# Kernel optimization log

Hardware: AMD Instinct MI355X
Metric: run time of the kernel (lower is better)

Reference implementation:

```python
import jax, jax.numpy as jnp
import numpy as np

B, S, D_MODEL, N_HEADS = 2, 256, 512, 8
HEAD_DIM = D_MODEL // N_HEADS  # 64; k.size(-1) used for scaling


def setup_inputs() -> dict:
    key = jax.random.key(0)
    ks = jax.random.split(key, 11)
    sd = 1.0 / np.sqrt(D_MODEL)
    sf = 1.0 / np.sqrt(N_HEADS * D_MODEL)
    return {
        "Q": jax.random.normal(ks[0], (B, S, D_MODEL), jnp.float32),
        "K": jax.random.normal(ks[1], (B, S, D_MODEL), jnp.float32),
        "V": jax.random.normal(ks[2], (B, S, D_MODEL), jnp.float32),
        "Wq": jax.random.normal(ks[3], (D_MODEL, D_MODEL * N_HEADS), jnp.float32) * sd,
        "bq": jax.random.normal(ks[4], (D_MODEL * N_HEADS,), jnp.float32) * sd,
        "Wk": jax.random.normal(ks[5], (D_MODEL, D_MODEL * N_HEADS), jnp.float32) * sd,
        "bk": jax.random.normal(ks[6], (D_MODEL * N_HEADS,), jnp.float32) * sd,
        "Wv": jax.random.normal(ks[7], (D_MODEL, D_MODEL * N_HEADS), jnp.float32) * sd,
        "bv": jax.random.normal(ks[8], (D_MODEL * N_HEADS,), jnp.float32) * sd,
        "Wf": jax.random.normal(ks[9], (N_HEADS * D_MODEL, D_MODEL), jnp.float32) * sf,
        "bf": jax.random.normal(ks[10], (D_MODEL,), jnp.float32) * sf,
    }


def _split_heads(x):
    # Faithful to torch: view(B, -1, n_heads, d_model//n_heads).transpose(1, 2).
    # x: (B, S, D_MODEL*N_HEADS) -> (B, N_HEADS, S*N_HEADS, HEAD_DIM)
    b = x.shape[0]
    return jnp.transpose(x.reshape(b, -1, N_HEADS, HEAD_DIM), (0, 2, 1, 3))


def reference(Q, K, V, Wq, bq, Wk, bk, Wv, bv, Wf, bf):
    q = _split_heads(Q @ Wq + bq)  # (B, H, S*H, Dh)
    k = _split_heads(K @ Wk + bk)
    v = _split_heads(V @ Wv + bv)
    scale = 1.0 / jnp.sqrt(jnp.float32(HEAD_DIM))
    scores = jnp.einsum("bhqd,bhkd->bhqk", q, k) * scale  # (B, H, S*H, S*H)
    weights = jax.nn.softmax(scores, axis=-1)
    ctx = jnp.einsum("bhqk,bhkd->bhqd", weights, v)  # (B, H, S*H, Dh)
    # transpose(1,2).view(B, -1, n_heads*d_model) -> (B, S, N_HEADS*D_MODEL)
    ctx = jnp.transpose(ctx, (0, 2, 1, 3)).reshape(Q.shape[0], -1, N_HEADS * D_MODEL)
    return ctx @ Wf + bf  # (B, S, D_MODEL)
```

## Files before the change

kernel.cpp:

```cpp
#include <hip/hip_runtime.h>
#include <hip/hip_bf16.h>


typedef __attribute__((ext_vector_type(4))) float f32x4;
typedef __attribute__((ext_vector_type(8))) short short8;
typedef __attribute__((ext_vector_type(4))) short short4v;

#define SEQ 2048
#define DH 64
#define BH 16
#define ROWS 512
#define DM 512
#define NQ 4096
#define KSPLIT 8

static __device__ __forceinline__ unsigned short f2bf(float f) {
    return __builtin_bit_cast(unsigned short, __float2bfloat16(f));
}
static __device__ __forceinline__ short4v pk4(float a, float b, float c, float d) {
    return short4v{(short)f2bf(a), (short)f2bf(b), (short)f2bf(c), (short)f2bf(d)};
}

__global__ __launch_bounds__(256, 2) void qkv_proj_kernel(
    const float* __restrict__ Q, const float* __restrict__ K, const float* __restrict__ V,
    const float* __restrict__ Wq, const float* __restrict__ bq,
    const float* __restrict__ Wk, const float* __restrict__ bk,
    const float* __restrict__ Wv, const float* __restrict__ bv,
    unsigned short* __restrict__ q_bf, unsigned short* __restrict__ k_bf,
    unsigned short* __restrict__ vT_bf)
{
    const int mat = blockIdx.z;
    const float* X    = (mat == 0) ? Q  : (mat == 1) ? K  : V;
    const float* W    = (mat == 0) ? Wq : (mat == 1) ? Wk : Wv;
    const float* bias = (mat == 0) ? bq : (mat == 1) ? bk : bv;

    const int n0 = blockIdx.x * 64;
    const int m0 = blockIdx.y * 128;
    const int tid = threadIdx.x;
    const int w = tid >> 6, l = tid & 63;
    const int lr = l & 15, lg = l >> 4;

    __shared__ unsigned short a_lds[128][72];
    __shared__ unsigned short wt_lds[64 * 72];

    const int xr0 = tid >> 4, xc4 = (tid & 15) * 4;
    const int wn = tid & 63, wkseg = tid >> 6;
    const int wxr = (wn >> 3) & 7;

    f32x4 acc[2][4];
#pragma unroll
    for (int qh = 0; qh < 2; ++qh)
#pragma unroll
        for (int ct = 0; ct < 4; ++ct) acc[qh][ct] = f32x4{0.f, 0.f, 0.f, 0.f};

    float4 rx[8];
    float rwv[16];

#pragma unroll
    for (int i = 0; i < 8; ++i)
        rx[i] = *reinterpret_cast<const float4*>(X + (m0 + i * 16 + xr0) * DM + xc4);
#pragma unroll
    for (int j = 0; j < 16; ++j)
        rwv[j] = W[(size_t)(wkseg * 16 + j) * NQ + n0 + wn];

    for (int t = 0; t < 8; ++t) {
#pragma unroll
        for (int i = 0; i < 8; ++i)
            *reinterpret_cast<short4v*>(&a_lds[i * 16 + xr0][xc4]) =
                pk4(rx[i].x, rx[i].y, rx[i].z, rx[i].w);
#pragma unroll
        for (int j4 = 0; j4 < 4; ++j4) {
            int kb = wkseg * 2 + (j4 >> 1);
            int off = wn * 72 + ((kb ^ wxr) << 3) + (j4 & 1) * 4;
            *reinterpret_cast<short4v*>(&wt_lds[off]) =
                pk4(rwv[j4 * 4 + 0], rwv[j4 * 4 + 1], rwv[j4 * 4 + 2], rwv[j4 * 4 + 3]);
        }
        __syncthreads();

        if (t < 7) {
            int k0 = (t + 1) * 64;
#pragma unroll
            for (int i = 0; i < 8; ++i)
                rx[i] = *reinterpret_cast<const float4*>(X + (m0 + i * 16 + xr0) * DM + k0 + xc4);
#pragma unroll
            for (int j = 0; j < 16; ++j)
                rwv[j] = W[(size_t)(k0 + wkseg * 16 + j) * NQ + n0 + wn];
        }

#pragma unroll
        for (int ks = 0; ks < 2; ++ks) {
            short8 aA = *reinterpret_cast<const short8*>(&a_lds[w * 32 + lr][ks * 32 + lg * 8]);
            short8 aB = *reinterpret_cast<const short8*>(&a_lds[w * 32 + 16 + lr][ks * 32 + lg * 8]);
#pragma unroll
            for (int ct = 0; ct < 4; ++ct) {
                int row = ct * 16 + lr;
                int kb = ks * 4 + lg;
                short8 b = *reinterpret_cast<const short8*>(
                    &wt_lds[row * 72 + ((kb ^ ((row >> 3) & 7)) << 3)]);
                acc[0][ct] = __builtin_amdgcn_mfma_f32_16x16x32_bf16(aA, b, acc[0][ct], 0, 0, 0);
                acc[1][ct] = __builtin_amdgcn_mfma_f32_16x16x32_bf16(aB, b, acc[1][ct], 0, 0, 0);
            }
        }
        __syncthreads();
    }

#pragma unroll
    for (int ct = 0; ct < 4; ++ct) {
        int c = n0 + ct * 16 + lr;
        float bv_ = bias[c];
        int h = (c >> 6) & 7, d = c & 63, c1 = c >> 9;
#pragma unroll
        for (int qh = 0; qh < 2; ++qh)
#pragma unroll
            for (int r = 0; r < 4; ++r) {
                int row = m0 + w * 32 + qh * 16 + lg * 4 + r;
                int b = row >> 8, s = row & 255;
                int n = s * 8 + c1;
                unsigned short bfv = f2bf(acc[qh][ct][r] + bv_);
                if (mat == 0)      q_bf[((b * 8 + h) * SEQ + n) * DH + d] = bfv;
                else if (mat == 1) k_bf[((b * 8 + h) * SEQ + n) * DH + d] = bfv;
                else               vT_bf[((b * 8 + h) * DH + d) * SEQ + n] = bfv;
            }
    }
}

__global__ __launch_bounds__(512, 4) void attn_kernel(
    const unsigned short* __restrict__ q_bf,
    const unsigned short* __restrict__ k_bf,
    const unsigned short* __restrict__ vT_bf,
    unsigned short* __restrict__ ctx_bf)
{
    const int bh = blockIdx.y;
    const int b = bh >> 3, h = bh & 7;
    const int n0 = blockIdx.x * 64;
    const int tid = threadIdx.x;
    const int w = tid >> 6, l = tid & 63;
    const int wq = w & 3, half = w >> 2;
    const int lr = l & 15, lg = l >> 4;
    const int gtid = tid & 255;

    const unsigned short* qb = q_bf + (size_t)bh * SEQ * DH;
    const unsigned short* kb = k_bf + (size_t)bh * SEQ * DH;
    const unsigned short* vb = vT_bf + (size_t)bh * DH * SEQ;

    __shared__ unsigned short kl[2][64][72];
    __shared__ unsigned short vl[2][64][72];
    __shared__ unsigned short pl[8][16][72];
    __shared__ float o_lds[4][16][68];
    __shared__ float l_lds[4][16];

    const int qrow = n0 + wq * 16 + lr;
    short8 aq[2];
    aq[0] = *reinterpret_cast<const short8*>(qb + qrow * DH + lg * 8);
    aq[1] = *reinterpret_cast<const short8*>(qb + qrow * DH + 32 + lg * 8);

    f32x4 o[4];
    float l_part[4];
#pragma unroll
    for (int i = 0; i < 4; ++i) {
        o[i] = f32x4{0.f, 0.f, 0.f, 0.f};
        l_part[i] = 0.f;
    }

    const int srow = gtid >> 3, sc8 = (gtid & 7) * 8;
    const int kbase0 = half * (SEQ / 2);

    short8 rk[2], rv[2];
#pragma unroll
    for (int i = 0; i < 2; ++i) {
        int row = srow + i * 32;
        rk[i] = *reinterpret_cast<const short8*>(kb + (kbase0 + row) * DH + sc8);
        rv[i] = *reinterpret_cast<const short8*>(vb + row * SEQ + kbase0 + sc8);
    }

    for (int kt = 0; kt < SEQ / 2 / 64; ++kt) {
#pragma unroll
        for (int i = 0; i < 2; ++i) {
            *reinterpret_cast<short8*>(&kl[half][srow + i * 32][sc8]) = rk[i];
            *reinterpret_cast<short8*>(&vl[half][srow + i * 32][sc8]) = rv[i];
        }
        __syncthreads();

        if (kt < SEQ / 2 / 64 - 1) {
            int kb0 = kbase0 + (kt + 1) * 64;
#pragma unroll
            for (int i = 0; i < 2; ++i) {
                int row = srow + i * 32;
                rk[i] = *reinterpret_cast<const short8*>(kb + (kb0 + row) * DH + sc8);
                rv[i] = *reinterpret_cast<const short8*>(vb + row * SEQ + kb0 + sc8);
            }
        }

        f32x4 s[4];
#pragma unroll
        for (int ct = 0; ct < 4; ++ct) s[ct] = f32x4{0.f, 0.f, 0.f, 0.f};
#pragma unroll
        for (int ks = 0; ks < 2; ++ks) {
#pragma unroll
            for (int ct = 0; ct < 4; ++ct) {
                short8 bfrag = *reinterpret_cast<const short8*>(&kl[half][ct * 16 + lr][ks * 32 + lg * 8]);
                s[ct] = __builtin_amdgcn_mfma_f32_16x16x32_bf16(aq[ks], bfrag, s[ct], 0, 0, 0);
            }
        }

#pragma unroll
        for (int r = 0; r < 4; ++r) {
            float rs = 0.f;
#pragma unroll
            for (int ct = 0; ct < 4; ++ct) {
                float p = __expf(s[ct][r] * 0.125f);
                s[ct][r] = p;
                rs += p;
            }
            l_part[r] += rs;
#pragma unroll
            for (int ct = 0; ct < 4; ++ct)
                pl[w][lg * 4 + r][ct * 16 + lr] = f2bf(s[ct][r]);
        }
        asm volatile("s_waitcnt lgkmcnt(0)" ::: "memory");
        __builtin_amdgcn_sched_barrier(0);

#pragma unroll
        for (int ks = 0; ks < 2; ++ks) {
            short8 pa = *reinterpret_cast<const short8*>(&pl[w][lr][ks * 32 + lg * 8]);
#pragma unroll
            for (int dt = 0; dt < 4; ++dt) {
                short8 vfrag = *reinterpret_cast<const short8*>(&vl[half][dt * 16 + lr][ks * 32 + lg * 8]);
                o[dt] = __builtin_amdgcn_mfma_f32_16x16x32_bf16(pa, vfrag, o[dt], 0, 0, 0);
            }
        }
        __syncthreads();
    }

    float lsum[4];
#pragma unroll
    for (int r = 0; r < 4; ++r) {
        float rs = l_part[r];
        rs += __shfl_xor(rs, 1);
        rs += __shfl_xor(rs, 2);
        rs += __shfl_xor(rs, 4);
        rs += __shfl_xor(rs, 8);
        lsum[r] = rs;
    }

    if (half == 1) {
#pragma unroll
        for (int r = 0; r < 4; ++r) {
#pragma unroll
            for (int dt = 0; dt < 4; ++dt)
                o_lds[wq][lg * 4 + r][dt * 16 + lr] = o[dt][r];
            if (lr == 0) l_lds[wq][lg * 4 + r] = lsum[r];
        }
    }
    __syncthreads();
    if (half == 0) {
#pragma unroll
        for (int r = 0; r < 4; ++r) {
            float l_tot = lsum[r] + l_lds[wq][lg * 4 + r];
            float inv = 1.f / l_tot;
            int n = n0 + wq * 16 + lg * 4 + r;
            int sp = n >> 3;
            int cbase = (n & 7) * 512 + h * 64;
#pragma unroll
            for (int dt = 0; dt < 4; ++dt) {
                float ot = o[dt][r] + o_lds[wq][lg * 4 + r][dt * 16 + lr];
                ctx_bf[((size_t)(b * 256 + sp)) * NQ + cbase + dt * 16 + lr] = f2bf(ot * inv);
            }
        }
    }
}

__global__ __launch_bounds__(256) void out_proj_splitk_kernel(
    const unsigned short* __restrict__ ctx_bf,
    const float* __restrict__ Wf,
    float* __restrict__ part)
{
    const int n0 = blockIdx.x * 64;
    const int m0 = blockIdx.y * 64;
    const int ksplit = blockIdx.z;
    const int kbase = ksplit * (NQ / KSPLIT);
    const int tid = threadIdx.x;
    const int w = tid >> 6, l = tid & 63;
    const int lr = l & 15, lg = l >> 4;

    __shared__ unsigned short a_lds[64][72];
    __shared__ unsigned short wt_lds[64 * 72];

    const int arow0 = tid >> 3, ac8 = (tid & 7) * 8;
    const int wn = tid & 63, wkseg = tid >> 6;
    const int wxr = (wn >> 3) & 7;

    f32x4 acc[4];
#pragma unroll
    for (int ct = 0; ct < 4; ++ct) acc[ct] = f32x4{0.f, 0.f, 0.f, 0.f};

    short8 ra[2];
    float rwv[16];

    {
#pragma unroll
        for (int i = 0; i < 2; ++i)
            ra[i] = *reinterpret_cast<const short8*>(
                ctx_bf + (size_t)(m0 + arow0 + i * 32) * NQ + kbase + ac8);
#pragma unroll
        for (int j = 0; j < 16; ++j)
            rwv[j] = Wf[(size_t)(kbase + wkseg * 16 + j) * DM + n0 + wn];
    }

    for (int t = 0; t < 8; ++t) {
#pragma unroll
        for (int i = 0; i < 2; ++i)
            *reinterpret_cast<short8*>(&a_lds[arow0 + i * 32][ac8]) = ra[i];
#pragma unroll
        for (int j4 = 0; j4 < 4; ++j4) {
            int kb = wkseg * 2 + (j4 >> 1);
            int off = wn * 72 + ((kb ^ wxr) << 3) + (j4 & 1) * 4;
            *reinterpret_cast<short4v*>(&wt_lds[off]) =
                pk4(rwv[j4 * 4 + 0], rwv[j4 * 4 + 1], rwv[j4 * 4 + 2], rwv[j4 * 4 + 3]);
        }
        __syncthreads();

        if (t < 7) {
            int k0 = kbase + (t + 1) * 64;
#pragma unroll
            for (int i = 0; i < 2; ++i)
                ra[i] = *reinterpret_cast<const short8*>(
                    ctx_bf + (size_t)(m0 + arow0 + i * 32) * NQ + k0 + ac8);
#pragma unroll
            for (int j = 0; j < 16; ++j)
                rwv[j] = Wf[(size_t)(k0 + wkseg * 16 + j) * DM + n0 + wn];
        }

#pragma unroll
        for (int ks = 0; ks < 2; ++ks) {
            short8 a = *reinterpret_cast<const short8*>(&a_lds[w * 16 + lr][ks * 32 + lg * 8]);
#pragma unroll
            for (int ct = 0; ct < 4; ++ct) {
                int row = ct * 16 + lr;
                int kb = ks * 4 + lg;
                short8 b = *reinterpret_cast<const short8*>(
                    &wt_lds[row * 72 + ((kb ^ ((row >> 3) & 7)) << 3)]);
                acc[ct] = __builtin_amdgcn_mfma_f32_16x16x32_bf16(a, b, acc[ct], 0, 0, 0);
            }
        }
        __syncthreads();
    }

    float* pbase = part + (size_t)ksplit * ROWS * DM;
#pragma unroll
    for (int ct = 0; ct < 4; ++ct) {
        int c = n0 + ct * 16 + lr;
#pragma unroll
        for (int r = 0; r < 4; ++r) {
            int row = m0 + w * 16 + lg * 4 + r;
            pbase[(size_t)row * DM + c] = acc[ct][r];
        }
    }
}

__global__ __launch_bounds__(256) void out_reduce_kernel(
    const float* __restrict__ part, const float* __restrict__ bf_,
    float* __restrict__ out)
{
    int i4 = blockIdx.x * 256 + threadIdx.x;
    int e = i4 * 4;
    float4 acc = *reinterpret_cast<const float4*>(bf_ + (e & (DM - 1)));
#pragma unroll
    for (int ks = 0; ks < KSPLIT; ++ks) {
        float4 p = *reinterpret_cast<const float4*>(part + (size_t)ks * ROWS * DM + e);
        acc.x += p.x; acc.y += p.y; acc.z += p.z; acc.w += p.w;
    }
    *reinterpret_cast<float4*>(out + e) = acc;
}

extern "C" void kernel_launch(void* const* d_in, const int* in_sizes, int n_in,
                              void* d_out, int out_size, void* d_ws, size_t ws_size,
                              hipStream_t stream) {
    const float* Q  = (const float*)d_in[0];
    const float* K  = (const float*)d_in[1];
    const float* V  = (const float*)d_in[2];
    const float* Wq = (const float*)d_in[3];
    const float* bq = (const float*)d_in[4];
    const float* Wk = (const float*)d_in[5];
    const float* bk = (const float*)d_in[6];
    const float* Wv = (const float*)d_in[7];
    const float* bv = (const float*)d_in[8];
    const float* Wf = (const float*)d_in[9];
    const float* bf = (const float*)d_in[10];
    float* out = (float*)d_out;

    unsigned short* q_bf  = (unsigned short*)d_ws;
    unsigned short* k_bf  = q_bf + (size_t)BH * SEQ * DH;
    unsigned short* vT_bf = k_bf + (size_t)BH * SEQ * DH;
    unsigned short* ctx_bf = vT_bf + (size_t)BH * SEQ * DH;
    float* part = (float*)d_ws;

    qkv_proj_kernel<<<dim3(NQ / 64, ROWS / 128, 3), 256, 0, stream>>>(
        Q, K, V, Wq, bq, Wk, bk, Wv, bv, q_bf, k_bf, vT_bf);
    attn_kernel<<<dim3(SEQ / 64, BH), 512, 0, stream>>>(q_bf, k_bf, vT_bf, ctx_bf);
    out_proj_splitk_kernel<<<dim3(DM / 64, ROWS / 64, KSPLIT), 256, 0, stream>>>(
        ctx_bf, Wf, part);
    out_reduce_kernel<<<dim3(ROWS * DM / 4 / 256), 256, 0, stream>>>(part, bf, out);
}
```

Baseline: 78.97 us.

## Enlarge out-proj M tile, add adaptive split-K, and prioritize MFMA waves in attention

```diff
diff --git a/kernel.cpp b/kernel.cpp
--- a/kernel.cpp
+++ b/kernel.cpp
@@ -12,7 +12,6 @@
 #define ROWS 512
 #define DM 512
 #define NQ 4096
-#define KSPLIT 8
 
 static __device__ __forceinline__ unsigned short f2bf(float f) {
     return __builtin_bit_cast(unsigned short, __float2bfloat16(f));
@@ -194,6 +193,7 @@
         f32x4 s[4];
 #pragma unroll
         for (int ct = 0; ct < 4; ++ct) s[ct] = f32x4{0.f, 0.f, 0.f, 0.f};
+        __builtin_amdgcn_s_setprio(1);
 #pragma unroll
         for (int ks = 0; ks < 2; ++ks) {
 #pragma unroll
@@ -202,6 +202,7 @@
                 s[ct] = __builtin_amdgcn_mfma_f32_16x16x32_bf16(aq[ks], bfrag, s[ct], 0, 0, 0);
             }
         }
+        __builtin_amdgcn_s_setprio(0);
 
 #pragma unroll
         for (int r = 0; r < 4; ++r) {
@@ -220,6 +221,7 @@
         asm volatile("s_waitcnt lgkmcnt(0)" ::: "memory");
         __builtin_amdgcn_sched_barrier(0);
 
+        __builtin_amdgcn_s_setprio(1);
 #pragma unroll
         for (int ks = 0; ks < 2; ++ks) {
             short8 pa = *reinterpret_cast<const short8*>(&pl[w][lr][ks * 32 + lg * 8]);
@@ -229,6 +231,7 @@
                 o[dt] = __builtin_amdgcn_mfma_f32_16x16x32_bf16(pa, vfrag, o[dt], 0, 0, 0);
             }
         }
+        __builtin_amdgcn_s_setprio(0);
         __syncthreads();
     }
 
@@ -270,36 +273,38 @@
     }
 }
 
-__global__ __launch_bounds__(256) void out_proj_splitk_kernel(
+__global__ __launch_bounds__(256, 2) void out_proj_splitk_kernel(
     const unsigned short* __restrict__ ctx_bf,
     const float* __restrict__ Wf,
-    float* __restrict__ part)
+    float* __restrict__ part, int iters)
 {
     const int n0 = blockIdx.x * 64;
-    const int m0 = blockIdx.y * 64;
+    const int m0 = blockIdx.y * 128;
     const int ksplit = blockIdx.z;
-    const int kbase = ksplit * (NQ / KSPLIT);
+    const int kbase = ksplit * (iters * 64);
     const int tid = threadIdx.x;
     const int w = tid >> 6, l = tid & 63;
     const int lr = l & 15, lg = l >> 4;
 
-    __shared__ unsigned short a_lds[64][72];
+    __shared__ unsigned short a_lds[128][72];
     __shared__ unsigned short wt_lds[64 * 72];
 
     const int arow0 = tid >> 3, ac8 = (tid & 7) * 8;
     const int wn = tid & 63, wkseg = tid >> 6;
     const int wxr = (wn >> 3) & 7;
 
-    f32x4 acc[4];
-#pragma unroll
-    for (int ct = 0; ct < 4; ++ct) acc[ct] = f32x4{0.f, 0.f, 0.f, 0.f};
-
-    short8 ra[2];
+    f32x4 acc[2][4];
+#pragma unroll
+    for (int qh = 0; qh < 2; ++qh)
+#pragma unroll
+        for (int ct = 0; ct < 4; ++ct) acc[qh][ct] = f32x4{0.f, 0.f, 0.f, 0.f};
+
+    short8 ra[4];
     float rwv[16];
 
     {
 #pragma unroll
-        for (int i = 0; i < 2; ++i)
+        for (int i = 0; i < 4; ++i)
             ra[i] = *reinterpret_cast<const short8*>(
                 ctx_bf + (size_t)(m0 + arow0 + i * 32) * NQ + kbase + ac8);
 #pragma unroll
@@ -307,9 +312,9 @@
             rwv[j] = Wf[(size_t)(kbase + wkseg * 16 + j) * DM + n0 + wn];
     }
 
-    for (int t = 0; t < 8; ++t) {
-#pragma unroll
-        for (int i = 0; i < 2; ++i)
+    for (int t = 0; t < iters; ++t) {
+#pragma unroll
+        for (int i = 0; i < 4; ++i)
             *reinterpret_cast<short8*>(&a_lds[arow0 + i * 32][ac8]) = ra[i];
 #pragma unroll
         for (int j4 = 0; j4 < 4; ++j4) {
@@ -320,10 +325,10 @@
         }
         __syncthreads();
 
-        if (t < 7) {
+        if (t < iters - 1) {
             int k0 = kbase + (t + 1) * 64;
 #pragma unroll
-            for (int i = 0; i < 2; ++i)
+            for (int i = 0; i < 4; ++i)
                 ra[i] = *reinterpret_cast<const short8*>(
                     ctx_bf + (size_t)(m0 + arow0 + i * 32) * NQ + k0 + ac8);
 #pragma unroll
@@ -333,14 +338,16 @@
 
 #pragma unroll
         for (int ks = 0; ks < 2; ++ks) {
-            short8 a = *reinterpret_cast<const short8*>(&a_lds[w * 16 + lr][ks * 32 + lg * 8]);
+            short8 aA = *reinterpret_cast<const short8*>(&a_lds[w * 32 + lr][ks * 32 + lg * 8]);
+            short8 aB = *reinterpret_cast<const short8*>(&a_lds[w * 32 + 16 + lr][ks * 32 + lg * 8]);
 #pragma unroll
             for (int ct = 0; ct < 4; ++ct) {
                 int row = ct * 16 + lr;
                 int kb = ks * 4 + lg;
                 short8 b = *reinterpret_cast<const short8*>(
                     &wt_lds[row * 72 + ((kb ^ ((row >> 3) & 7)) << 3)]);
-                acc[ct] = __builtin_amdgcn_mfma_f32_16x16x32_bf16(a, b, acc[ct], 0, 0, 0);
+                acc[0][ct] = __builtin_amdgcn_mfma_f32_16x16x32_bf16(aA, b, acc[0][ct], 0, 0, 0);
+                acc[1][ct] = __builtin_amdgcn_mfma_f32_16x16x32_bf16(aB, b, acc[1][ct], 0, 0, 0);
             }
         }
         __syncthreads();
@@ -351,22 +358,23 @@
     for (int ct = 0; ct < 4; ++ct) {
         int c = n0 + ct * 16 + lr;
 #pragma unroll
-        for (int r = 0; r < 4; ++r) {
-            int row = m0 + w * 16 + lg * 4 + r;
-            pbase[(size_t)row * DM + c] = acc[ct][r];
-        }
+        for (int qh = 0; qh < 2; ++qh)
+#pragma unroll
+            for (int r = 0; r < 4; ++r) {
+                int row = m0 + w * 32 + qh * 16 + lg * 4 + r;
+                pbase[(size_t)row * DM + c] = acc[qh][ct][r];
+            }
     }
 }
 
 __global__ __launch_bounds__(256) void out_reduce_kernel(
     const float* __restrict__ part, const float* __restrict__ bf_,
-    float* __restrict__ out)
+    float* __restrict__ out, int nsplit)
 {
     int i4 = blockIdx.x * 256 + threadIdx.x;
     int e = i4 * 4;
     float4 acc = *reinterpret_cast<const float4*>(bf_ + (e & (DM - 1)));
-#pragma unroll
-    for (int ks = 0; ks < KSPLIT; ++ks) {
+    for (int ks = 0; ks < nsplit; ++ks) {
         float4 p = *reinterpret_cast<const float4*>(part + (size_t)ks * ROWS * DM + e);
         acc.x += p.x; acc.y += p.y; acc.z += p.z; acc.w += p.w;
     }
@@ -393,12 +401,17 @@
     unsigned short* k_bf  = q_bf + (size_t)BH * SEQ * DH;
     unsigned short* vT_bf = k_bf + (size_t)BH * SEQ * DH;
     unsigned short* ctx_bf = vT_bf + (size_t)BH * SEQ * DH;
-    float* part = (float*)d_ws;
+
+    const size_t MB16 = (size_t)16 * 1024 * 1024;
+    const bool big = ws_size >= MB16 * 2;
+    float* part = big ? (float*)((char*)d_ws + MB16) : (float*)d_ws;
+    const int nsplit = big ? 16 : 8;
+    const int iters  = big ? 4 : 8;
 
     qkv_proj_kernel<<<dim3(NQ / 64, ROWS / 128, 3), 256, 0, stream>>>(
         Q, K, V, Wq, bq, Wk, bk, Wv, bv, q_bf, k_bf, vT_bf);
     attn_kernel<<<dim3(SEQ / 64, BH), 512, 0, stream>>>(q_bf, k_bf, vT_bf, ctx_bf);
-    out_proj_splitk_kernel<<<dim3(DM / 64, ROWS / 64, KSPLIT), 256, 0, stream>>>(
-        ctx_bf, Wf, part);
-    out_reduce_kernel<<<dim3(ROWS * DM / 4 / 256), 256, 0, stream>>>(part, bf, out);
-}
+    out_proj_splitk_kernel<<<dim3(DM / 64, ROWS / 128, nsplit), 256, 0, stream>>>(
+        ctx_bf, Wf, part, iters);
+    out_reduce_kernel<<<dim3(ROWS * DM / 4 / 256), 256, 0, stream>>>(part, bf, out, nsplit);
+}
```

After: 82.52 us. 4.5% more time.
